# Kernel optimization log

Measured on AMD Instinct MI355X. Metric: run time of the kernel, lower is better.

The kernel has to match this reference:

```python
import jax, jax.numpy as jnp
import numpy as np

E = 1024   # embed_dim
H = 16     # num_heads
D = E // H # head_dim
BS = 512   # block_size
G = 128    # global_len
B = 1
S = 8192


def setup_inputs() -> dict:
    key = jax.random.key(0)
    ks = jax.random.split(key, 7)
    w_scale = 0.02
    return {
        "token_hidden_states": jax.random.normal(ks[0], (B, S, E), jnp.float32),
        "global_hidden_states": jax.random.normal(ks[1], (B, G, E), jnp.float32),
        "attention_mask": jnp.zeros((B, S), jnp.float32),  # additive float mask
        "Wq": jax.random.normal(ks[2], (E, E), jnp.float32) * w_scale,
        "Wk": jax.random.normal(ks[3], (E, E), jnp.float32) * w_scale,
        "Wv": jax.random.normal(ks[4], (E, E), jnp.float32) * w_scale,
        "Wo": jax.random.normal(ks[5], (E, E), jnp.float32) * w_scale,
    }


def _shape(x):
    # [B, L, E] -> [B, H, L, D]
    b, l, _ = x.shape
    return x.reshape(b, l, H, D).transpose(0, 2, 1, 3)


def reference(token_hidden_states, global_hidden_states, attention_mask, Wq, Wk, Wv, Wo):
    b, s, _ = token_hidden_states.shape
    g = global_hidden_states.shape[1]
    n = s // BS  # num_blocks
    scaling = D ** -0.5

    local_q = _shape(token_hidden_states @ Wq * scaling)
    local_k = _shape(token_hidden_states @ Wk)
    local_v = _shape(token_hidden_states @ Wv)
    global_q = _shape(global_hidden_states @ Wq * scaling)
    global_k = _shape(global_hidden_states @ Wk)
    global_v = _shape(global_hidden_states @ Wv)

    # ---- global attention: global queries attend to [global + all local] keys
    k_cat = jnp.concatenate([global_k, local_k], axis=2)   # [B,H,G+S,D]
    v_cat = jnp.concatenate([global_v, local_v], axis=2)
    ext_mask = jnp.pad(attention_mask, ((0, 0), (g, 0)))    # [B,G+S]
    gw = jnp.einsum('bhgf,bhxf->bhgx', global_q, k_cat) + ext_mask[:, None, None, :]
    gp = jax.nn.softmax(gw, axis=-1)
    g_out = jnp.einsum('bhgx,bhxf->bhgf', gp, v_cat)        # [B,H,G,D]
    g_out = g_out.transpose(0, 2, 1, 3).reshape(b, g, E) @ Wo

    # ---- local attention: block-local + global keys
    bq = local_q.reshape(b, H, n, BS, D)
    bk = local_k.reshape(b, H, n, BS, D)
    bv = local_v.reshape(b, H, n, BS, D)
    ext_mask_l = jnp.pad(attention_mask.reshape(b, n, BS), ((0, 0), (0, 0), (g, 0)))  # [B,N,G+K]
    l2g = jnp.einsum('bhnkf,bhgf->bhnkg', bq, global_k)     # [B,H,N,K,G]
    l2l = jnp.einsum('bhnkf,bhnxf->bhnkx', bq, bk)          # [B,H,N,K,K]
    lw = jnp.concatenate([l2g, l2l], axis=-1) + ext_mask_l[:, None, :, None, :]
    lp = jax.nn.softmax(lw, axis=-1)
    l_out = (jnp.einsum('bhnkg,bhgf->bhnkf', lp[..., :g], global_v)
             + jnp.einsum('bhnkx,bhnxf->bhnkf', lp[..., g:], bv))  # [B,H,N,K,D]
    l_out = l_out.transpose(0, 2, 3, 1, 4).reshape(b, s, E) @ Wo

    return (l_out, g_out)
```

## Files before the change

### kernel.cpp

```cpp
#include <hip/hip_runtime.h>
#include <stdint.h>

#define S_LEN  8192
#define G_LEN  128
#define E_DIM  1024
#define H_NUM  16
#define BS_LEN 512
#define R_TOT  8320
#define KBLK   128
#define XBLK   1040
#define NSPL   10
#define SPLW   832

typedef _Float16 half8    __attribute__((ext_vector_type(8)));
typedef _Float16 half4    __attribute__((ext_vector_type(4)));
typedef float    floatx4  __attribute__((ext_vector_type(4)));
typedef float    floatx16 __attribute__((ext_vector_type(16)));

#define QSCALE 0.18033688011112042f

#define OFF_XP   0
#define OFF_AOP  0
#define OFF_WP   17039360
#define SZ_WP1   2097152
#define OFF_QP   25427968
#define OFF_KP   42467328
#define OFF_VP   59506688
#define OFF_FH   76546048
#define OFF_OG   76579328
#define OFF_LG   81822208

__device__ __forceinline__ floatx16 zero16() {
  floatx16 v;
#pragma unroll
  for (int i = 0; i < 16; ++i) v[i] = 0.0f;
  return v;
}
__device__ __forceinline__ floatx4 zero4() {
  floatx4 v;
#pragma unroll
  for (int i = 0; i < 4; ++i) v[i] = 0.0f;
  return v;
}

__device__ __forceinline__ void gl_lds16(const void* g, void* l) {
  __builtin_amdgcn_global_load_lds(
      (const __attribute__((address_space(1))) void*)g,
      (__attribute__((address_space(3))) void*)l, 16, 0, 0);
}

__device__ __forceinline__ int pk_f16x2(float a, float b) {
  return __builtin_bit_cast(int, __builtin_amdgcn_cvt_pkrtz(a, b));
}

__global__ __launch_bounds__(256) void pack_x_k(const float* __restrict__ tok,
                                                const float* __restrict__ glob,
                                                char* __restrict__ ws) {
  __shared__ __align__(16) _Float16 tile[64 * 132];
  const int tid = threadIdx.x;
  const int r0 = blockIdx.y * 64;
  const int c0 = blockIdx.x * 128;
#pragma unroll
  for (int kk = 0; kk < 8; ++kk) {
    int f   = tid + kk * 256;
    int row = f >> 5;
    int c4  = (f & 31) * 4;
    int r   = r0 + row;
    const float* src = (r < G_LEN) ? glob + (size_t)r * E_DIM
                                   : tok + (size_t)(r - G_LEN) * E_DIM;
    float4 v = *(const float4*)&src[c0 + c4];
    half4 h;
    h[0] = (_Float16)v.x; h[1] = (_Float16)v.y; h[2] = (_Float16)v.z; h[3] = (_Float16)v.w;
    *(half4*)&tile[row * 132 + c4] = h;
  }
  __syncthreads();
  _Float16* Xp = (_Float16*)(ws + OFF_XP);
#pragma unroll
  for (int uu = 0; uu < 4; ++uu) {
    int u    = tid + uu * 256;
    int kb_l = u >> 6;
    int row  = u & 63;
    half4 a = *(const half4*)&tile[row * 132 + kb_l * 8];
    half4 b = *(const half4*)&tile[row * 132 + kb_l * 8 + 4];
    half8 o;
    o[0] = a[0]; o[1] = a[1]; o[2] = a[2]; o[3] = a[3];
    o[4] = b[0]; o[5] = b[1]; o[6] = b[2]; o[7] = b[3];
    int kb = (c0 >> 3) + kb_l;
    *(half8*)&Xp[((size_t)kb * R_TOT + r0 + row) * 8] = o;
  }
}

__global__ void pack_w_k(const float* __restrict__ Wq, const float* __restrict__ Wk,
                         const float* __restrict__ Wv, const float* __restrict__ Wo,
                         const float* __restrict__ mask, char* __restrict__ ws) {
  int t = blockIdx.x * 256 + threadIdx.x;
  const int NW = 4 * KBLK * 1024;
  if (t < NW) {
    int w   = t >> 17;
    int rem = t & 131071;
    int kb  = rem >> 10;
    int n   = rem & 1023;
    const float* W = (w == 0) ? Wq : (w == 1) ? Wk : (w == 2) ? Wv : Wo;
    half8 v;
#pragma unroll
    for (int j = 0; j < 8; ++j)
      v[j] = (_Float16)W[(size_t)(kb * 8 + j) * 1024 + n];
    *(half8*)(ws + OFF_WP + (size_t)w * SZ_WP1 + (size_t)(kb * 1024 + n) * 16) = v;
  } else {
    int t2 = t - NW;
    if (t2 < R_TOT) {
      _Float16* fh = (_Float16*)(ws + OFF_FH);
      float m = (t2 < G_LEN) ? 0.0f : mask[t2 - G_LEN];
      fh[t2] = (_Float16)__expf(m);
    }
  }
}

template <bool SWAP>
__device__ __forceinline__ void gemm_tile(const _Float16* __restrict__ Ap,
                                          const _Float16* __restrict__ Bp,
                                          int m0, int n0, _Float16* lds,
                                          floatx4 acc[4][4]) {
  const int tid  = threadIdx.x;
  const int wave = tid >> 6;
  const int lane = tid & 63;
  const int quad = lane >> 4;
  const int l16  = lane & 15;
  _Float16* As = lds;
  _Float16* Bs = lds + 8 * 128 * 8;
  const int wm = (wave >> 1) * 64;
  const int wn = (wave & 1) * 64;
  for (int step = 0; step < 16; ++step) {
#pragma unroll
    for (int ui = 0; ui < 8; ++ui) {
      const int u   = wave * 8 + ui;
      const int isB = u >> 4;
      const int vv  = u & 15;
      const int kb  = vv >> 1;
      const int rh  = vv & 1;
      const _Float16* src =
          isB ? Bp + (size_t)((step * 8 + kb) * 1024 + n0 + rh * 64 + lane) * 8
              : Ap + (size_t)((step * 8 + kb) * R_TOT + m0 + rh * 64 + lane) * 8;
      _Float16* dst = (isB ? Bs : As) + (kb * 128 + rh * 64) * 8;
      gl_lds16(src, dst);
    }
    __syncthreads();
#pragma unroll
    for (int kk = 0; kk < 2; ++kk) {
      half8 af[4], bf[4];
#pragma unroll
      for (int mt = 0; mt < 4; ++mt)
        af[mt] = *(const half8*)(As + ((kk * 4 + quad) * 128 + wm + mt * 16 + l16) * 8);
#pragma unroll
      for (int nt = 0; nt < 4; ++nt)
        bf[nt] = *(const half8*)(Bs + ((kk * 4 + quad) * 128 + wn + nt * 16 + l16) * 8);
#pragma unroll
      for (int mt = 0; mt < 4; ++mt)
#pragma unroll
        for (int nt = 0; nt < 4; ++nt)
          acc[mt][nt] = SWAP
            ? __builtin_amdgcn_mfma_f32_16x16x32_f16(bf[nt], af[mt], acc[mt][nt], 0, 0, 0)
            : __builtin_amdgcn_mfma_f32_16x16x32_f16(af[mt], bf[nt], acc[mt][nt], 0, 0, 0);
    }
    __syncthreads();
  }
}

__global__ __launch_bounds__(256) void qk_gemm_k(char* __restrict__ ws) {
  __shared__ __align__(16) _Float16 lds[2 * 8 * 128 * 8];
  const int z  = blockIdx.z;
  const int m0 = blockIdx.y * 128;
  const int n0 = blockIdx.x * 128;
  floatx4 acc[4][4];
#pragma unroll
  for (int a = 0; a < 4; ++a)
#pragma unroll
    for (int b = 0; b < 4; ++b) acc[a][b] = zero4();
  gemm_tile<true>((const _Float16*)(ws + OFF_XP),
                  (const _Float16*)(ws + OFF_WP + (size_t)z * SZ_WP1), m0, n0, lds, acc);
  _Float16* dst = (_Float16*)(ws + (z == 0 ? OFF_QP : OFF_KP));
  const int lane = threadIdx.x & 63, wave = threadIdx.x >> 6;
  const int quad = lane >> 4, l16 = lane & 15;
  const int wm = (wave >> 1) * 64, wn = (wave & 1) * 64;
  const float scale = (z == 0) ? QSCALE : 1.0f;
#pragma unroll
  for (int mt = 0; mt < 4; ++mt)
#pragma unroll
    for (int nt = 0; nt < 4; ++nt) {
      int m  = m0 + wm + mt * 16 + l16;
      int nb = n0 + wn + nt * 16 + quad * 4;
      half4 h;
#pragma unroll
      for (int r = 0; r < 4; ++r) h[r] = (_Float16)(acc[mt][nt][r] * scale);
      int db = (nb >> 6) * 8 + ((nb & 63) >> 3);
      *(half4*)&dst[((size_t)db * R_TOT + m) * 8 + (nb & 7)] = h;
    }
}

__global__ __launch_bounds__(256) void v_gemm_k(char* __restrict__ ws) {
  __shared__ __align__(16) _Float16 lds[2 * 8 * 128 * 8];
  const int m0 = blockIdx.y * 128;
  const int n0 = blockIdx.x * 128;
  floatx4 acc[4][4];
#pragma unroll
  for (int a = 0; a < 4; ++a)
#pragma unroll
    for (int b = 0; b < 4; ++b) acc[a][b] = zero4();
  gemm_tile<false>((const _Float16*)(ws + OFF_XP),
                   (const _Float16*)(ws + OFF_WP + 2 * (size_t)SZ_WP1), m0, n0, lds, acc);
  _Float16* dst = (_Float16*)(ws + OFF_VP);
  const _Float16* fh = (const _Float16*)(ws + OFF_FH);
  const int lane = threadIdx.x & 63, wave = threadIdx.x >> 6;
  const int quad = lane >> 4, l16 = lane & 15;
  const int wm = (wave >> 1) * 64, wn = (wave & 1) * 64;
#pragma unroll
  for (int mt = 0; mt < 4; ++mt)
#pragma unroll
    for (int nt = 0; nt < 4; ++nt) {
      int mb = m0 + wm + mt * 16 + quad * 4;
      int n  = n0 + wn + nt * 16 + l16;
      half4 fv = *(const half4*)&fh[mb];
      half4 h;
#pragma unroll
      for (int r = 0; r < 4; ++r) h[r] = (_Float16)(acc[mt][nt][r] * (float)fv[r]);
      *(half4*)&dst[(((size_t)(n >> 6) * XBLK + (mb >> 3)) * 64 + (n & 63)) * 8 + (mb & 7)] = h;
    }
}

__device__ __forceinline__ void attn_chunks(const _Float16* __restrict__ Kph,
                                            const _Float16* __restrict__ Vph,
                                            const _Float16* __restrict__ fh,
                                            const half8 qa[4], int lane,
                                            int kbase0, int nch,
                                            floatx16& o0, floatx16& o1, floatx16& lacc) {
  const int  half_ = lane >> 5;
  const int  c     = lane & 31;
  const bool hb    = half_ != 0;
  for (int ci = 0; ci < nch; ++ci) {
    const int kb = kbase0 + ci * 32;
    floatx16 s = zero16();
#pragma unroll
    for (int ks = 0; ks < 4; ++ks) {
      half8 kfr = *(const half8*)&Kph[(size_t)((ks * 2 + half_) * R_TOT + kb + c) * 8];
      s = __builtin_amdgcn_mfma_f32_32x32x16_f16(kfr, qa[ks], s, 0, 0, 0);
    }
    int pk[8];
#pragma unroll
    for (int i = 0; i < 8; ++i) {
      float e0 = __builtin_amdgcn_exp2f(s[2 * i]);
      float e1 = __builtin_amdgcn_exp2f(s[2 * i + 1]);
      pk[i] = pk_f16x2(e0, e1);
    }
    int sw[8];
#pragma unroll
    for (int i = 0; i < 8; ++i) sw[i] = __shfl_xor(pk[i], 32);
    int4 bi0, bi1;
    bi0.x = hb ? sw[2] : pk[0];  bi0.y = hb ? sw[3] : pk[1];
    bi0.z = hb ? pk[2] : sw[0];  bi0.w = hb ? pk[3] : sw[1];
    bi1.x = hb ? sw[6] : pk[4];  bi1.y = hb ? sw[7] : pk[5];
    bi1.z = hb ? pk[6] : sw[4];  bi1.w = hb ? pk[7] : sw[5];
    half8 b0 = __builtin_bit_cast(half8, bi0);
    half8 b1 = __builtin_bit_cast(half8, bi1);
    half8 f0 = *(const half8*)&fh[kb + half_ * 8];
    half8 f1 = *(const half8*)&fh[kb + 16 + half_ * 8];
    lacc = __builtin_amdgcn_mfma_f32_32x32x16_f16(f0, b0, lacc, 0, 0, 0);
    lacc = __builtin_amdgcn_mfma_f32_32x32x16_f16(f1, b1, lacc, 0, 0, 0);
    const int xb = kb >> 3;
    half8 vA0 = *(const half8*)&Vph[(size_t)((xb + half_) * 64 + c) * 8];
    half8 vA1 = *(const half8*)&Vph[(size_t)((xb + 2 + half_) * 64 + c) * 8];
    half8 vB0 = *(const half8*)&Vph[(size_t)((xb + half_) * 64 + 32 + c) * 8];
    half8 vB1 = *(const half8*)&Vph[(size_t)((xb + 2 + half_) * 64 + 32 + c) * 8];
    o0 = __builtin_amdgcn_mfma_f32_32x32x16_f16(vA0, b0, o0, 0, 0, 0);
    o0 = __builtin_amdgcn_mfma_f32_32x32x16_f16(vA1, b1, o0, 0, 0, 0);
    o1 = __builtin_amdgcn_mfma_f32_32x32x16_f16(vB0, b0, o1, 0, 0, 0);
    o1 = __builtin_amdgcn_mfma_f32_32x32x16_f16(vB1, b1, o1, 0, 0, 0);
  }
}

__global__ __launch_bounds__(256) void local_attn_k(char* __restrict__ ws) {
  const int wave = threadIdx.x >> 6, lane = threadIdx.x & 63;
  const int h = blockIdx.z, blk = blockIdx.y, qg = blockIdx.x;
  const int qbase = G_LEN + blk * BS_LEN + qg * 128 + wave * 32;
  const _Float16* Qph = (const _Float16*)(ws + OFF_QP) + (size_t)h * 8 * R_TOT * 8;
  const _Float16* Kph = (const _Float16*)(ws + OFF_KP) + (size_t)h * 8 * R_TOT * 8;
  const _Float16* Vph = (const _Float16*)(ws + OFF_VP) + (size_t)h * XBLK * 64 * 8;
  const _Float16* fh  = (const _Float16*)(ws + OFF_FH);
  const int half_ = lane >> 5, c = lane & 31;
  half8 qa[4];
#pragma unroll
  for (int ks = 0; ks < 4; ++ks)
    qa[ks] = *(const half8*)&Qph[(size_t)((ks * 2 + half_) * R_TOT + qbase + c) * 8];
  floatx16 o0 = zero16(), o1 = zero16(), l = zero16();
  attn_chunks(Kph, Vph, fh, qa, lane, 0, G_LEN / 32, o0, o1, l);
  attn_chunks(Kph, Vph, fh, qa, lane, G_LEN + blk * BS_LEN, BS_LEN / 32, o0, o1, l);
  _Float16* AOp = (_Float16*)(ws + OFF_AOP);
  const float inv = 1.0f / l[0];
  const int m = qbase + c;
#pragma unroll
  for (int g = 0; g < 4; ++g) {
    half4 ha, hc;
#pragma unroll
    for (int i = 0; i < 4; ++i) {
      ha[i] = (_Float16)(o0[4 * g + i] * inv);
      hc[i] = (_Float16)(o1[4 * g + i] * inv);
    }
    *(half4*)&AOp[((size_t)(h * 8 + g) * R_TOT + m) * 8 + 4 * half_] = ha;
    *(half4*)&AOp[((size_t)(h * 8 + 4 + g) * R_TOT + m) * 8 + 4 * half_] = hc;
  }
}

__global__ __launch_bounds__(256) void global_attn_k(char* __restrict__ ws) {
  const int wave = threadIdx.x >> 6, lane = threadIdx.x & 63;
  const int spl = blockIdx.x, h = blockIdx.y;
  const int qbase = wave * 32;
  const _Float16* Qph = (const _Float16*)(ws + OFF_QP) + (size_t)h * 8 * R_TOT * 8;
  const _Float16* Kph = (const _Float16*)(ws + OFF_KP) + (size_t)h * 8 * R_TOT * 8;
  const _Float16* Vph = (const _Float16*)(ws + OFF_VP) + (size_t)h * XBLK * 64 * 8;
  const _Float16* fh  = (const _Float16*)(ws + OFF_FH);
  const int half_ = lane >> 5, c = lane & 31;
  half8 qa[4];
#pragma unroll
  for (int ks = 0; ks < 4; ++ks)
    qa[ks] = *(const half8*)&Qph[(size_t)((ks * 2 + half_) * R_TOT + qbase + c) * 8];
  floatx16 o0 = zero16(), o1 = zero16(), l = zero16();
  attn_chunks(Kph, Vph, fh, qa, lane, spl * SPLW, SPLW / 32, o0, o1, l);
  float* Og = (float*)(ws + OFF_OG);
  float* Lg = (float*)(ws + OFF_LG);
  const int q = qbase + c;
#pragma unroll
  for (int g = 0; g < 4; ++g) {
    float4 fa, fb;
    fa.x = o0[4 * g]; fa.y = o0[4 * g + 1]; fa.z = o0[4 * g + 2]; fa.w = o0[4 * g + 3];
    fb.x = o1[4 * g]; fb.y = o1[4 * g + 1]; fb.z = o1[4 * g + 2]; fb.w = o1[4 * g + 3];
    *(float4*)&Og[((size_t)(spl * H_NUM + h) * 128 + q) * 64 + 8 * g + 4 * half_] = fa;
    *(float4*)&Og[((size_t)(spl * H_NUM + h) * 128 + q) * 64 + 32 + 8 * g + 4 * half_] = fb;
  }
  if (half_ == 0) Lg[(spl * H_NUM + h) * 128 + q] = l[0];
}

__global__ void combine_k(char* __restrict__ ws) {
  int idx = blockIdx.x * 256 + threadIdx.x;
  int h = idx >> 13, rem = idx & 8191, q = rem >> 6, d = rem & 63;
  const float* Og = (const float*)(ws + OFF_OG);
  const float* Lg = (const float*)(ws + OFF_LG);
  float o = 0.0f, l = 0.0f;
#pragma unroll
  for (int s = 0; s < NSPL; ++s) {
    o += Og[(size_t)((s * H_NUM + h) * 128 + q) * 64 + d];
    l += Lg[(s * H_NUM + h) * 128 + q];
  }
  int n = h * 64 + d;
  ((_Float16*)(ws + OFF_AOP))[((size_t)(n >> 3) * R_TOT + q) * 8 + (n & 7)] = (_Float16)(o / l);
}

__global__ __launch_bounds__(256) void out_gemm_k(char* __restrict__ ws, float* __restrict__ dout) {
  __shared__ __align__(16) _Float16 lds[2 * 8 * 128 * 8];
  const int m0 = blockIdx.y * 128;
  const int n0 = blockIdx.x * 128;
  floatx4 acc[4][4];
#pragma unroll
  for (int a = 0; a < 4; ++a)
#pragma unroll
    for (int b = 0; b < 4; ++b) acc[a][b] = zero4();
  gemm_tile<true>((const _Float16*)(ws + OFF_AOP),
                  (const _Float16*)(ws + OFF_WP + 3 * (size_t)SZ_WP1), m0, n0, lds, acc);
  const int lane = threadIdx.x & 63, wave = threadIdx.x >> 6;
  const int quad = lane >> 4, l16 = lane & 15;
  const int wm = (wave >> 1) * 64, wn = (wave & 1) * 64;
#pragma unroll
  for (int mt = 0; mt < 4; ++mt)
#pragma unroll
    for (int nt = 0; nt < 4; ++nt) {
      int m  = m0 + wm + mt * 16 + l16;
      int nb = n0 + wn + nt * 16 + quad * 4;
      float4 f4;
      f4.x = acc[mt][nt][0]; f4.y = acc[mt][nt][1];
      f4.z = acc[mt][nt][2]; f4.w = acc[mt][nt][3];
      float* p = (m < G_LEN) ? (dout + (size_t)S_LEN * E_DIM + (size_t)m * E_DIM + nb)
                             : (dout + (size_t)(m - G_LEN) * E_DIM + nb);
      *(float4*)p = f4;
    }
}

extern "C" void kernel_launch(void* const* d_in, const int* in_sizes, int n_in,
                              void* d_out, int out_size, void* d_ws, size_t ws_size,
                              hipStream_t stream) {
  const float* tok  = (const float*)d_in[0];
  const float* glob = (const float*)d_in[1];
  const float* mask = (const float*)d_in[2];
  const float* Wq   = (const float*)d_in[3];
  const float* Wk   = (const float*)d_in[4];
  const float* Wv   = (const float*)d_in[5];
  const float* Wo   = (const float*)d_in[6];
  char*  ws   = (char*)d_ws;
  float* dout = (float*)d_out;

  pack_x_k<<<dim3(8, 130), dim3(256), 0, stream>>>(tok, glob, ws);
  pack_w_k<<<dim3((4 * KBLK * 1024 + R_TOT + 255) / 256), dim3(256), 0, stream>>>(Wq, Wk, Wv, Wo, mask, ws);
  qk_gemm_k<<<dim3(8, 65, 2), dim3(256), 0, stream>>>(ws);
  v_gemm_k<<<dim3(8, 65), dim3(256), 0, stream>>>(ws);
  local_attn_k<<<dim3(4, 16, 16), dim3(256), 0, stream>>>(ws);
  global_attn_k<<<dim3(NSPL, H_NUM), dim3(256), 0, stream>>>(ws);
  combine_k<<<dim3(512), dim3(256), 0, stream>>>(ws);
  out_gemm_k<<<dim3(8, 65), dim3(256), 0, stream>>>(ws, dout);
}
```

Baseline: 313.0 us.

## Merge kernel launches and load GEMM A operand directly from global memory

Measured after the change: 324.1 us. 1.04x slower.

```diff
diff --git a/kernel.cpp b/kernel.cpp
--- a/kernel.cpp
+++ b/kernel.cpp
@@ -53,96 +53,92 @@
   return __builtin_bit_cast(int, __builtin_amdgcn_cvt_pkrtz(a, b));
 }
 
-__global__ __launch_bounds__(256) void pack_x_k(const float* __restrict__ tok,
-                                                const float* __restrict__ glob,
-                                                char* __restrict__ ws) {
+__global__ __launch_bounds__(256) void prep_k(const float* __restrict__ tok,
+                                              const float* __restrict__ glob,
+                                              const float* __restrict__ Wq,
+                                              const float* __restrict__ Wk,
+                                              const float* __restrict__ Wv,
+                                              const float* __restrict__ Wo,
+                                              const float* __restrict__ mask,
+                                              char* __restrict__ ws) {
   __shared__ __align__(16) _Float16 tile[64 * 132];
+  const int bx  = blockIdx.x;
   const int tid = threadIdx.x;
-  const int r0 = blockIdx.y * 64;
-  const int c0 = blockIdx.x * 128;
-#pragma unroll
-  for (int kk = 0; kk < 8; ++kk) {
-    int f   = tid + kk * 256;
-    int row = f >> 5;
-    int c4  = (f & 31) * 4;
-    int r   = r0 + row;
-    const float* src = (r < G_LEN) ? glob + (size_t)r * E_DIM
-                                   : tok + (size_t)(r - G_LEN) * E_DIM;
-    float4 v = *(const float4*)&src[c0 + c4];
-    half4 h;
-    h[0] = (_Float16)v.x; h[1] = (_Float16)v.y; h[2] = (_Float16)v.z; h[3] = (_Float16)v.w;
-    *(half4*)&tile[row * 132 + c4] = h;
-  }
-  __syncthreads();
-  _Float16* Xp = (_Float16*)(ws + OFF_XP);
-#pragma unroll
-  for (int uu = 0; uu < 4; ++uu) {
-    int u    = tid + uu * 256;
-    int kb_l = u >> 6;
-    int row  = u & 63;
-    half4 a = *(const half4*)&tile[row * 132 + kb_l * 8];
-    half4 b = *(const half4*)&tile[row * 132 + kb_l * 8 + 4];
-    half8 o;
-    o[0] = a[0]; o[1] = a[1]; o[2] = a[2]; o[3] = a[3];
-    o[4] = b[0]; o[5] = b[1]; o[6] = b[2]; o[7] = b[3];
-    int kb = (c0 >> 3) + kb_l;
-    *(half8*)&Xp[((size_t)kb * R_TOT + r0 + row) * 8] = o;
-  }
-}
-
-__global__ void pack_w_k(const float* __restrict__ Wq, const float* __restrict__ Wk,
-                         const float* __restrict__ Wv, const float* __restrict__ Wo,
-                         const float* __restrict__ mask, char* __restrict__ ws) {
-  int t = blockIdx.x * 256 + threadIdx.x;
-  const int NW = 4 * KBLK * 1024;
-  if (t < NW) {
-    int w   = t >> 17;
-    int rem = t & 131071;
-    int kb  = rem >> 10;
-    int n   = rem & 1023;
-    const float* W = (w == 0) ? Wq : (w == 1) ? Wk : (w == 2) ? Wv : Wo;
-    half8 v;
-#pragma unroll
-    for (int j = 0; j < 8; ++j)
-      v[j] = (_Float16)W[(size_t)(kb * 8 + j) * 1024 + n];
-    *(half8*)(ws + OFF_WP + (size_t)w * SZ_WP1 + (size_t)(kb * 1024 + n) * 16) = v;
+  if (bx < 1040) {
+    const int r0 = (bx >> 3) * 64;
+    const int c0 = (bx & 7) * 128;
+#pragma unroll
+    for (int kk = 0; kk < 8; ++kk) {
+      int f   = tid + kk * 256;
+      int row = f >> 5;
+      int c4  = (f & 31) * 4;
+      int r   = r0 + row;
+      const float* src = (r < G_LEN) ? glob + (size_t)r * E_DIM
+                                     : tok + (size_t)(r - G_LEN) * E_DIM;
+      float4 v = *(const float4*)&src[c0 + c4];
+      half4 h;
+      h[0] = (_Float16)v.x; h[1] = (_Float16)v.y; h[2] = (_Float16)v.z; h[3] = (_Float16)v.w;
+      *(half4*)&tile[row * 132 + c4] = h;
+    }
+    __syncthreads();
+    _Float16* Xp = (_Float16*)(ws + OFF_XP);
+#pragma unroll
+    for (int uu = 0; uu < 4; ++uu) {
+      int u    = tid + uu * 256;
+      int kb_l = u >> 6;
+      int row  = u & 63;
+      half4 a = *(const half4*)&tile[row * 132 + kb_l * 8];
+      half4 b = *(const half4*)&tile[row * 132 + kb_l * 8 + 4];
+      half8 o;
+      o[0] = a[0]; o[1] = a[1]; o[2] = a[2]; o[3] = a[3];
+      o[4] = b[0]; o[5] = b[1]; o[6] = b[2]; o[7] = b[3];
+      int kb = (c0 >> 3) + kb_l;
+      *(half8*)&Xp[((size_t)kb * R_TOT + r0 + row) * 8] = o;
+    }
   } else {
-    int t2 = t - NW;
-    if (t2 < R_TOT) {
-      _Float16* fh = (_Float16*)(ws + OFF_FH);
-      float m = (t2 < G_LEN) ? 0.0f : mask[t2 - G_LEN];
-      fh[t2] = (_Float16)__expf(m);
-    }
-  }
-}
-
-template <bool SWAP>
-__device__ __forceinline__ void gemm_tile(const _Float16* __restrict__ Ap,
-                                          const _Float16* __restrict__ Bp,
-                                          int m0, int n0, _Float16* lds,
-                                          floatx4 acc[4][4]) {
+    int t = (bx - 1040) * 256 + tid;
+    const int NW = 4 * KBLK * 1024;
+    if (t < NW) {
+      int w   = t >> 17;
+      int rem = t & 131071;
+      int kb  = rem >> 10;
+      int n   = rem & 1023;
+      const float* W = (w == 0) ? Wq : (w == 1) ? Wk : (w == 2) ? Wv : Wo;
+      half8 v;
+#pragma unroll
+      for (int j = 0; j < 8; ++j)
+        v[j] = (_Float16)W[(size_t)(kb * 8 + j) * 1024 + n];
+      *(half8*)(ws + OFF_WP + (size_t)w * SZ_WP1 + (size_t)(kb * 1024 + n) * 16) = v;
+    } else {
+      int t2 = t - NW;
+      if (t2 < R_TOT) {
+        _Float16* fh = (_Float16*)(ws + OFF_FH);
+        float m = (t2 < G_LEN) ? 0.0f : mask[t2 - G_LEN];
+        fh[t2] = (_Float16)__expf(m);
+      }
+    }
+  }
+}
+
+__device__ __forceinline__ void gemm_mainloop(const _Float16* __restrict__ Ap,
+                                              const _Float16* __restrict__ Bp,
+                                              int m0, int n0, _Float16* Bs,
+                                              floatx4 acc[4][4]) {
   const int tid  = threadIdx.x;
   const int wave = tid >> 6;
   const int lane = tid & 63;
   const int quad = lane >> 4;
   const int l16  = lane & 15;
-  _Float16* As = lds;
-  _Float16* Bs = lds + 8 * 128 * 8;
   const int wm = (wave >> 1) * 64;
   const int wn = (wave & 1) * 64;
   for (int step = 0; step < 16; ++step) {
 #pragma unroll
-    for (int ui = 0; ui < 8; ++ui) {
-      const int u   = wave * 8 + ui;
-      const int isB = u >> 4;
-      const int vv  = u & 15;
-      const int kb  = vv >> 1;
-      const int rh  = vv & 1;
-      const _Float16* src =
-          isB ? Bp + (size_t)((step * 8 + kb) * 1024 + n0 + rh * 64 + lane) * 8
-              : Ap + (size_t)((step * 8 + kb) * R_TOT + m0 + rh * 64 + lane) * 8;
-      _Float16* dst = (isB ? Bs : As) + (kb * 128 + rh * 64) * 8;
-      gl_lds16(src, dst);
+    for (int ui = 0; ui < 4; ++ui) {
+      const int u  = wave * 4 + ui;
+      const int kb = u >> 1;
+      const int rh = u & 1;
+      const _Float16* src = Bp + (size_t)((step * 8 + kb) * 1024 + n0 + rh * 64 + lane) * 8;
+      gl_lds16(src, Bs + (kb * 128 + rh * 64) * 8);
     }
     __syncthreads();
 #pragma unroll
@@ -150,7 +146,7 @@
       half8 af[4], bf[4];
 #pragma unroll
       for (int mt = 0; mt < 4; ++mt)
-        af[mt] = *(const half8*)(As + ((kk * 4 + quad) * 128 + wm + mt * 16 + l16) * 8);
+        af[mt] = *(const half8*)&Ap[(size_t)((step * 8 + kk * 4 + quad) * R_TOT + m0 + wm + mt * 16 + l16) * 8];
 #pragma unroll
       for (int nt = 0; nt < 4; ++nt)
         bf[nt] = *(const half8*)(Bs + ((kk * 4 + quad) * 128 + wn + nt * 16 + l16) * 8);
@@ -158,73 +154,63 @@
       for (int mt = 0; mt < 4; ++mt)
 #pragma unroll
         for (int nt = 0; nt < 4; ++nt)
-          acc[mt][nt] = SWAP
-            ? __builtin_amdgcn_mfma_f32_16x16x32_f16(bf[nt], af[mt], acc[mt][nt], 0, 0, 0)
-            : __builtin_amdgcn_mfma_f32_16x16x32_f16(af[mt], bf[nt], acc[mt][nt], 0, 0, 0);
+          acc[mt][nt] = __builtin_amdgcn_mfma_f32_16x16x32_f16(bf[nt], af[mt], acc[mt][nt], 0, 0, 0);
     }
     __syncthreads();
   }
 }
 
-__global__ __launch_bounds__(256) void qk_gemm_k(char* __restrict__ ws) {
-  __shared__ __align__(16) _Float16 lds[2 * 8 * 128 * 8];
-  const int z  = blockIdx.z;
+__global__ __launch_bounds__(256) void qkv_gemm_k(char* __restrict__ ws) {
+  __shared__ __align__(16) _Float16 Bs[8 * 128 * 8];
+  const int z  = blockIdx.x >> 3;
+  const int n0 = (blockIdx.x & 7) * 128;
   const int m0 = blockIdx.y * 128;
-  const int n0 = blockIdx.x * 128;
   floatx4 acc[4][4];
 #pragma unroll
   for (int a = 0; a < 4; ++a)
 #pragma unroll
     for (int b = 0; b < 4; ++b) acc[a][b] = zero4();
-  gemm_tile<true>((const _Float16*)(ws + OFF_XP),
-                  (const _Float16*)(ws + OFF_WP + (size_t)z * SZ_WP1), m0, n0, lds, acc);
-  _Float16* dst = (_Float16*)(ws + (z == 0 ? OFF_QP : OFF_KP));
+  gemm_mainloop((const _Float16*)(ws + OFF_XP),
+                (const _Float16*)(ws + OFF_WP + (size_t)z * SZ_WP1), m0, n0, Bs, acc);
+
   const int lane = threadIdx.x & 63, wave = threadIdx.x >> 6;
   const int quad = lane >> 4, l16 = lane & 15;
   const int wm = (wave >> 1) * 64, wn = (wave & 1) * 64;
-  const float scale = (z == 0) ? QSCALE : 1.0f;
-#pragma unroll
-  for (int mt = 0; mt < 4; ++mt)
-#pragma unroll
-    for (int nt = 0; nt < 4; ++nt) {
-      int m  = m0 + wm + mt * 16 + l16;
-      int nb = n0 + wn + nt * 16 + quad * 4;
-      half4 h;
-#pragma unroll
-      for (int r = 0; r < 4; ++r) h[r] = (_Float16)(acc[mt][nt][r] * scale);
-      int db = (nb >> 6) * 8 + ((nb & 63) >> 3);
-      *(half4*)&dst[((size_t)db * R_TOT + m) * 8 + (nb & 7)] = h;
-    }
-}
-
-__global__ __launch_bounds__(256) void v_gemm_k(char* __restrict__ ws) {
-  __shared__ __align__(16) _Float16 lds[2 * 8 * 128 * 8];
-  const int m0 = blockIdx.y * 128;
-  const int n0 = blockIdx.x * 128;
-  floatx4 acc[4][4];
-#pragma unroll
-  for (int a = 0; a < 4; ++a)
-#pragma unroll
-    for (int b = 0; b < 4; ++b) acc[a][b] = zero4();
-  gemm_tile<false>((const _Float16*)(ws + OFF_XP),
-                   (const _Float16*)(ws + OFF_WP + 2 * (size_t)SZ_WP1), m0, n0, lds, acc);
-  _Float16* dst = (_Float16*)(ws + OFF_VP);
   const _Float16* fh = (const _Float16*)(ws + OFF_FH);
-  const int lane = threadIdx.x & 63, wave = threadIdx.x >> 6;
-  const int quad = lane >> 4, l16 = lane & 15;
-  const int wm = (wave >> 1) * 64, wn = (wave & 1) * 64;
-#pragma unroll
-  for (int mt = 0; mt < 4; ++mt)
-#pragma unroll
-    for (int nt = 0; nt < 4; ++nt) {
-      int mb = m0 + wm + mt * 16 + quad * 4;
-      int n  = n0 + wn + nt * 16 + l16;
-      half4 fv = *(const half4*)&fh[mb];
-      half4 h;
-#pragma unroll
-      for (int r = 0; r < 4; ++r) h[r] = (_Float16)(acc[mt][nt][r] * (float)fv[r]);
-      *(half4*)&dst[(((size_t)(n >> 6) * XBLK + (mb >> 3)) * 64 + (n & 63)) * 8 + (mb & 7)] = h;
-    }
+  if (z < 2) {
+    _Float16* dst = (_Float16*)(ws + (z == 0 ? OFF_QP : OFF_KP));
+    const float scale = (z == 0) ? QSCALE : 1.0f;
+#pragma unroll
+    for (int mt = 0; mt < 4; ++mt)
+#pragma unroll
+      for (int nt = 0; nt < 4; ++nt) {
+        int m  = m0 + wm + mt * 16 + l16;
+        int nb = n0 + wn + nt * 16 + quad * 4;
+        half4 h;
+#pragma unroll
+        for (int r = 0; r < 4; ++r) h[r] = (_Float16)(acc[mt][nt][r] * scale);
+        int db = (nb >> 6) * 8 + ((nb & 63) >> 3);
+        *(half4*)&dst[((size_t)db * R_TOT + m) * 8 + (nb & 7)] = h;
+      }
+  } else {
+    _Float16* dst = (_Float16*)(ws + OFF_VP);
+#pragma unroll
+    for (int mt = 0; mt < 4; ++mt) {
+      int m = m0 + wm + mt * 16 + l16;
+      float fhm = (float)fh[m];
+#pragma unroll
+      for (int nt = 0; nt < 4; ++nt) {
+        int nb = wn + nt * 16 + quad * 4;
+        int nl = (n0 & 1023) + nb;
+#pragma unroll
+        for (int r = 0; r < 4; ++r) {
+          int n = nl + r;
+          dst[(((size_t)(n >> 6) * XBLK + (m >> 3)) * 64 + (n & 63)) * 8 + (m & 7)] =
+              (_Float16)(acc[mt][nt][r] * fhm);
+        }
+      }
+    }
+  }
 }
 
 __device__ __forceinline__ void attn_chunks(const _Float16* __restrict__ Kph,
@@ -277,65 +263,64 @@
   }
 }
 
-__global__ __launch_bounds__(256) void local_attn_k(char* __restrict__ ws) {
+__global__ __launch_bounds__(256) void attn_k(char* __restrict__ ws) {
   const int wave = threadIdx.x >> 6, lane = threadIdx.x & 63;
-  const int h = blockIdx.z, blk = blockIdx.y, qg = blockIdx.x;
-  const int qbase = G_LEN + blk * BS_LEN + qg * 128 + wave * 32;
-  const _Float16* Qph = (const _Float16*)(ws + OFF_QP) + (size_t)h * 8 * R_TOT * 8;
-  const _Float16* Kph = (const _Float16*)(ws + OFF_KP) + (size_t)h * 8 * R_TOT * 8;
-  const _Float16* Vph = (const _Float16*)(ws + OFF_VP) + (size_t)h * XBLK * 64 * 8;
-  const _Float16* fh  = (const _Float16*)(ws + OFF_FH);
+  const int bx = blockIdx.x;
+  const _Float16* fh = (const _Float16*)(ws + OFF_FH);
   const int half_ = lane >> 5, c = lane & 31;
-  half8 qa[4];
-#pragma unroll
-  for (int ks = 0; ks < 4; ++ks)
-    qa[ks] = *(const half8*)&Qph[(size_t)((ks * 2 + half_) * R_TOT + qbase + c) * 8];
-  floatx16 o0 = zero16(), o1 = zero16(), l = zero16();
-  attn_chunks(Kph, Vph, fh, qa, lane, 0, G_LEN / 32, o0, o1, l);
-  attn_chunks(Kph, Vph, fh, qa, lane, G_LEN + blk * BS_LEN, BS_LEN / 32, o0, o1, l);
-  _Float16* AOp = (_Float16*)(ws + OFF_AOP);
-  const float inv = 1.0f / l[0];
-  const int m = qbase + c;
-#pragma unroll
-  for (int g = 0; g < 4; ++g) {
-    half4 ha, hc;
-#pragma unroll
-    for (int i = 0; i < 4; ++i) {
-      ha[i] = (_Float16)(o0[4 * g + i] * inv);
-      hc[i] = (_Float16)(o1[4 * g + i] * inv);
-    }
-    *(half4*)&AOp[((size_t)(h * 8 + g) * R_TOT + m) * 8 + 4 * half_] = ha;
-    *(half4*)&AOp[((size_t)(h * 8 + 4 + g) * R_TOT + m) * 8 + 4 * half_] = hc;
-  }
-}
-
-__global__ __launch_bounds__(256) void global_attn_k(char* __restrict__ ws) {
-  const int wave = threadIdx.x >> 6, lane = threadIdx.x & 63;
-  const int spl = blockIdx.x, h = blockIdx.y;
-  const int qbase = wave * 32;
-  const _Float16* Qph = (const _Float16*)(ws + OFF_QP) + (size_t)h * 8 * R_TOT * 8;
-  const _Float16* Kph = (const _Float16*)(ws + OFF_KP) + (size_t)h * 8 * R_TOT * 8;
-  const _Float16* Vph = (const _Float16*)(ws + OFF_VP) + (size_t)h * XBLK * 64 * 8;
-  const _Float16* fh  = (const _Float16*)(ws + OFF_FH);
-  const int half_ = lane >> 5, c = lane & 31;
-  half8 qa[4];
-#pragma unroll
-  for (int ks = 0; ks < 4; ++ks)
-    qa[ks] = *(const half8*)&Qph[(size_t)((ks * 2 + half_) * R_TOT + qbase + c) * 8];
-  floatx16 o0 = zero16(), o1 = zero16(), l = zero16();
-  attn_chunks(Kph, Vph, fh, qa, lane, spl * SPLW, SPLW / 32, o0, o1, l);
-  float* Og = (float*)(ws + OFF_OG);
-  float* Lg = (float*)(ws + OFF_LG);
-  const int q = qbase + c;
-#pragma unroll
-  for (int g = 0; g < 4; ++g) {
-    float4 fa, fb;
-    fa.x = o0[4 * g]; fa.y = o0[4 * g + 1]; fa.z = o0[4 * g + 2]; fa.w = o0[4 * g + 3];
-    fb.x = o1[4 * g]; fb.y = o1[4 * g + 1]; fb.z = o1[4 * g + 2]; fb.w = o1[4 * g + 3];
-    *(float4*)&Og[((size_t)(spl * H_NUM + h) * 128 + q) * 64 + 8 * g + 4 * half_] = fa;
-    *(float4*)&Og[((size_t)(spl * H_NUM + h) * 128 + q) * 64 + 32 + 8 * g + 4 * half_] = fb;
-  }
-  if (half_ == 0) Lg[(spl * H_NUM + h) * 128 + q] = l[0];
+  if (bx < 1024) {
+    const int h = bx >> 6, blk = (bx >> 2) & 15, qg = bx & 3;
+    const int qbase = G_LEN + blk * BS_LEN + qg * 128 + wave * 32;
+    const _Float16* Qph = (const _Float16*)(ws + OFF_QP) + (size_t)h * 8 * R_TOT * 8;
+    const _Float16* Kph = (const _Float16*)(ws + OFF_KP) + (size_t)h * 8 * R_TOT * 8;
+    const _Float16* Vph = (const _Float16*)(ws + OFF_VP) + (size_t)h * XBLK * 64 * 8;
+    half8 qa[4];
+#pragma unroll
+    for (int ks = 0; ks < 4; ++ks)
+      qa[ks] = *(const half8*)&Qph[(size_t)((ks * 2 + half_) * R_TOT + qbase + c) * 8];
+    floatx16 o0 = zero16(), o1 = zero16(), l = zero16();
+    attn_chunks(Kph, Vph, fh, qa, lane, 0, G_LEN / 32, o0, o1, l);
+    attn_chunks(Kph, Vph, fh, qa, lane, G_LEN + blk * BS_LEN, BS_LEN / 32, o0, o1, l);
+    _Float16* AOp = (_Float16*)(ws + OFF_AOP);
+    const float inv = 1.0f / l[0];
+    const int m = qbase + c;
+#pragma unroll
+    for (int g = 0; g < 4; ++g) {
+      half4 ha, hc;
+#pragma unroll
+      for (int i = 0; i < 4; ++i) {
+        ha[i] = (_Float16)(o0[4 * g + i] * inv);
+        hc[i] = (_Float16)(o1[4 * g + i] * inv);
+      }
+      *(half4*)&AOp[((size_t)(h * 8 + g) * R_TOT + m) * 8 + 4 * half_] = ha;
+      *(half4*)&AOp[((size_t)(h * 8 + 4 + g) * R_TOT + m) * 8 + 4 * half_] = hc;
+    }
+  } else {
+    const int t = bx - 1024;
+    const int spl = t % NSPL, h = t / NSPL;
+    const int qbase = wave * 32;
+    const _Float16* Qph = (const _Float16*)(ws + OFF_QP) + (size_t)h * 8 * R_TOT * 8;
+    const _Float16* Kph = (const _Float16*)(ws + OFF_KP) + (size_t)h * 8 * R_TOT * 8;
+    const _Float16* Vph = (const _Float16*)(ws + OFF_VP) + (size_t)h * XBLK * 64 * 8;
+    half8 qa[4];
+#pragma unroll
+    for (int ks = 0; ks < 4; ++ks)
+      qa[ks] = *(const half8*)&Qph[(size_t)((ks * 2 + half_) * R_TOT + qbase + c) * 8];
+    floatx16 o0 = zero16(), o1 = zero16(), l = zero16();
+    attn_chunks(Kph, Vph, fh, qa, lane, spl * SPLW, SPLW / 32, o0, o1, l);
+    float* Og = (float*)(ws + OFF_OG);
+    float* Lg = (float*)(ws + OFF_LG);
+    const int q = qbase + c;
+#pragma unroll
+    for (int g = 0; g < 4; ++g) {
+      float4 fa, fb;
+      fa.x = o0[4 * g]; fa.y = o0[4 * g + 1]; fa.z = o0[4 * g + 2]; fa.w = o0[4 * g + 3];
+      fb.x = o1[4 * g]; fb.y = o1[4 * g + 1]; fb.z = o1[4 * g + 2]; fb.w = o1[4 * g + 3];
+      *(float4*)&Og[((size_t)(spl * H_NUM + h) * 128 + q) * 64 + 8 * g + 4 * half_] = fa;
+      *(float4*)&Og[((size_t)(spl * H_NUM + h) * 128 + q) * 64 + 32 + 8 * g + 4 * half_] = fb;
+    }
+    if (half_ == 0) Lg[(spl * H_NUM + h) * 128 + q] = l[0];
+  }
 }
 
 __global__ void combine_k(char* __restrict__ ws) {
@@ -354,7 +339,7 @@
 }
 
 __global__ __launch_bounds__(256) void out_gemm_k(char* __restrict__ ws, float* __restrict__ dout) {
-  __shared__ __align__(16) _Float16 lds[2 * 8 * 128 * 8];
+  __shared__ __align__(16) _Float16 Bs[8 * 128 * 8];
   const int m0 = blockIdx.y * 128;
   const int n0 = blockIdx.x * 128;
   floatx4 acc[4][4];
@@ -362,8 +347,8 @@
   for (int a = 0; a < 4; ++a)
 #pragma unroll
     for (int b = 0; b < 4; ++b) acc[a][b] = zero4();
-  gemm_tile<true>((const _Float16*)(ws + OFF_AOP),
-                  (const _Float16*)(ws + OFF_WP + 3 * (size_t)SZ_WP1), m0, n0, lds, acc);
+  gemm_mainloop((const _Float16*)(ws + OFF_AOP),
+                (const _Float16*)(ws + OFF_WP + 3 * (size_t)SZ_WP1), m0, n0, Bs, acc);
   const int lane = threadIdx.x & 63, wave = threadIdx.x >> 6;
   const int quad = lane >> 4, l16 = lane & 15;
   const int wm = (wave >> 1) * 64, wn = (wave & 1) * 64;
@@ -395,12 +380,9 @@
   char*  ws   = (char*)d_ws;
   float* dout = (float*)d_out;
 
-  pack_x_k<<<dim3(8, 130), dim3(256), 0, stream>>>(tok, glob, ws);
-  pack_w_k<<<dim3((4 * KBLK * 1024 + R_TOT + 255) / 256), dim3(256), 0, stream>>>(Wq, Wk, Wv, Wo, mask, ws);
-  qk_gemm_k<<<dim3(8, 65, 2), dim3(256), 0, stream>>>(ws);
-  v_gemm_k<<<dim3(8, 65), dim3(256), 0, stream>>>(ws);
-  local_attn_k<<<dim3(4, 16, 16), dim3(256), 0, stream>>>(ws);
-  global_attn_k<<<dim3(NSPL, H_NUM), dim3(256), 0, stream>>>(ws);
+  prep_k<<<dim3(1040 + 2081), dim3(256), 0, stream>>>(tok, glob, Wq, Wk, Wv, Wo, mask, ws);
+  qkv_gemm_k<<<dim3(24, 65), dim3(256), 0, stream>>>(ws);
+  attn_k<<<dim3(1024 + NSPL * H_NUM), dim3(256), 0, stream>>>(ws);
   combine_k<<<dim3(512), dim3(256), 0, stream>>>(ws);
   out_gemm_k<<<dim3(8, 65), dim3(256), 0, stream>>>(ws, dout);
 }
```
